# Optimization experiments

Measured on AMD Instinct MI355X. Metric: run time of the kernel, lower is better.

Reference implementation:

```python
import jax, jax.numpy as jnp
import numpy as np

HIDDEN = 1024
FFN = 4096
NUM_EXPERTS = 8
TOP_K = 2


def setup_inputs() -> dict:
    key = jax.random.key(0)
    k1, k2, k3, k4, k5 = jax.random.split(key, 5)
    B, T = 4, 2048
    x = jax.random.normal(k1, (B, T, HIDDEN), dtype=jnp.float32)
    # router: nn.Linear(hidden_dim, num_experts)
    bound = 1.0 / np.sqrt(HIDDEN)
    router_w = jax.random.uniform(k2, (NUM_EXPERTS, HIDDEN), dtype=jnp.float32, minval=-bound, maxval=bound)
    router_b = jax.random.uniform(k3, (NUM_EXPERTS,), dtype=jnp.float32, minval=-bound, maxval=bound)
    w1 = jax.random.normal(k4, (NUM_EXPERTS, HIDDEN, FFN), dtype=jnp.float32) * 0.02
    w2 = jax.random.normal(k5, (NUM_EXPERTS, FFN, HIDDEN), dtype=jnp.float32) * 0.02
    return {"x": x, "router_w": router_w, "router_b": router_b, "w1": w1, "w2": w2}


def reference(x, router_w, router_b, w1, w2):
    B, T, H = x.shape
    x_flat = x.reshape(-1, H)                      # [N, H], N = B*T
    logits = x_flat @ router_w.T + router_b        # [N, E]
    probs = jax.nn.softmax(logits, axis=-1)
    topk_w, topk_idx = jax.lax.top_k(probs, TOP_K)  # [N, K]
    topk_w = topk_w / jnp.sum(topk_w, axis=-1, keepdims=True)
    # combine weight per (expert, token): sum_k topk_w[:,k] * onehot(topk_idx[:,k])
    onehot = jax.nn.one_hot(topk_idx, NUM_EXPERTS, dtype=x.dtype)   # [N, K, E]
    combine = jnp.einsum('nk,nke->en', topk_w, onehot)              # [E, N]
    # dense per-expert FFN (math identical to original masked loop: gelu(0)=0)
    hidden = jax.nn.gelu(jnp.einsum('nh,ehf->enf', x_flat, w1), approximate=False)  # [E, N, F]
    expert_out = jnp.einsum('enf,efh->enh', hidden, w2)             # [E, N, H]
    out = jnp.einsum('enh,en->nh', expert_out, combine)             # [N, H]
    return out.reshape(B, T, H)
```

## Files before the change

### kernel.cpp

```cpp
#include <hip/hip_runtime.h>
#include <cstdint>
#include <cstddef>

#define H_DIM 1024
#define F_DIM 4096
#define N_EXP 8
#define N_TOK 8192
#define NK_ASSIGN (N_TOK * 2)
#define MAX_MB 24
#define NMB 32

typedef unsigned short u16;
typedef __attribute__((ext_vector_type(8))) short bf16x8;
typedef __attribute__((ext_vector_type(4))) float f32x4;

__device__ __forceinline__ u16 f2bf(float f) {
  unsigned int u = __float_as_uint(f);
  u += 0x7fffu + ((u >> 16) & 1u);
  return (u16)(u >> 16);
}

__device__ __forceinline__ void load16(const u16* g, u16* l) {
  __builtin_amdgcn_global_load_lds(
      (const __attribute__((address_space(1))) void*)g,
      (__attribute__((address_space(3))) void*)l, 16, 0, 0);
}

__global__ __launch_bounds__(256) void router_kernel(
    const float* __restrict__ x, const float* __restrict__ rw,
    const float* __restrict__ rb, int* __restrict__ topk_idx,
    float* __restrict__ topk_w, u16* __restrict__ xb) {
  const int lane = threadIdx.x & 63;
  const int wid = threadIdx.x >> 6;
  const int t = blockIdx.x * 4 + wid;
  const float4* xr = (const float4*)(x + (size_t)t * H_DIM);
  u16* xo = xb + (size_t)t * H_DIM;
  float acc[N_EXP];
#pragma unroll
  for (int e = 0; e < N_EXP; ++e) acc[e] = 0.f;
#pragma unroll
  for (int j = 0; j < 4; ++j) {
    float4 xv = xr[j * 64 + lane];
    ushort4 u;
    u.x = f2bf(xv.x); u.y = f2bf(xv.y); u.z = f2bf(xv.z); u.w = f2bf(xv.w);
    *(ushort4*)(xo + (size_t)(j * 64 + lane) * 4) = u;
#pragma unroll
    for (int e = 0; e < N_EXP; ++e) {
      float4 wv = ((const float4*)(rw + e * H_DIM))[j * 64 + lane];
      acc[e] += xv.x * wv.x + xv.y * wv.y + xv.z * wv.z + xv.w * wv.w;
    }
  }
#pragma unroll
  for (int off = 32; off > 0; off >>= 1) {
#pragma unroll
    for (int e = 0; e < N_EXP; ++e) acc[e] += __shfl_xor(acc[e], off);
  }
  if (lane == 0) {
    float lg[N_EXP];
#pragma unroll
    for (int e = 0; e < N_EXP; ++e) lg[e] = acc[e] + rb[e];
    int i0 = 0;
    float b0 = lg[0];
#pragma unroll
    for (int e = 1; e < N_EXP; ++e)
      if (lg[e] > b0) { b0 = lg[e]; i0 = e; }
    int i1 = -1;
    float b1 = -3.4e38f;
#pragma unroll
    for (int e = 0; e < N_EXP; ++e)
      if (e != i0 && lg[e] > b1) { b1 = lg[e]; i1 = e; }
    float w0 = 1.f / (1.f + __expf(b1 - b0));
    topk_idx[2 * t] = i0;
    topk_idx[2 * t + 1] = i1;
    topk_w[2 * t] = w0;
    topk_w[2 * t + 1] = 1.f - w0;
  }
}

__global__ __launch_bounds__(256) void hist_kernel(
    const int* __restrict__ topk_idx, int* __restrict__ hist_g) {
  __shared__ int hh[N_EXP];
  const int tid = threadIdx.x;
  if (tid < N_EXP) hh[tid] = 0;
  __syncthreads();
  const int t = blockIdx.x * 256 + tid;
  const int e0 = topk_idx[2 * t], e1 = topk_idx[2 * t + 1];
  atomicAdd(&hh[e0], 1);
  atomicAdd(&hh[e1], 1);
  __syncthreads();
  if (tid < N_EXP) hist_g[blockIdx.x * N_EXP + tid] = hh[tid];
}

__global__ __launch_bounds__(256) void scatter_kernel(
    const int* __restrict__ topk_idx, const float* __restrict__ topk_w,
    const int* __restrict__ hist_g, int* __restrict__ offsets,
    int* __restrict__ assign_token, float* __restrict__ assign_gate,
    int* __restrict__ slot_of) {
  __shared__ int sh[NMB * N_EXP];
  __shared__ int pb[N_EXP];
  __shared__ int cur[N_EXP];
  const int tid = threadIdx.x;
  sh[tid] = hist_g[tid];
  if (tid < N_EXP) cur[tid] = 0;
  __syncthreads();
  if (tid == 0) {
    int tot[N_EXP];
    for (int e = 0; e < N_EXP; ++e) tot[e] = 0;
    for (int b = 0; b < NMB; ++b)
      for (int e = 0; e < N_EXP; ++e) tot[e] += sh[b * N_EXP + e];
    int run = 0;
    for (int e = 0; e < N_EXP; ++e) {
      if (blockIdx.x == 0) offsets[e] = run;
      int r = run;
      for (int b = 0; b < (int)blockIdx.x; ++b) r += sh[b * N_EXP + e];
      pb[e] = r;
      run += tot[e];
    }
    if (blockIdx.x == 0) offsets[N_EXP] = run;
  }
  __syncthreads();
  const int t = blockIdx.x * 256 + tid;
#pragma unroll
  for (int k = 0; k < 2; ++k) {
    int e = topk_idx[2 * t + k];
    int local = atomicAdd(&cur[e], 1);
    int pos = pb[e] + local;
    assign_token[pos] = t;
    assign_gate[pos] = topk_w[2 * t + k];
    slot_of[2 * t + k] = pos;
  }
}

__global__ __launch_bounds__(256) void transpose_cvt(
    const float* __restrict__ in, u16* __restrict__ out, int R, int C) {
  __shared__ u16 lds[64 * 66];
  const int e = blockIdx.z;
  const float* ip = in + (size_t)e * R * C;
  u16* op = out + (size_t)e * R * C;
  const int c0 = blockIdx.x * 64, r0 = blockIdx.y * 64;
  const int tid = threadIdx.x;
  const int tx = tid & 15, ty = tid >> 4;
#pragma unroll
  for (int i = 0; i < 4; ++i) {
    const int r = ty + i * 16;
    float4 v = *(const float4*)(ip + (size_t)(r0 + r) * C + c0 + tx * 4);
    ushort2 u01, u23;
    u01.x = f2bf(v.x); u01.y = f2bf(v.y);
    u23.x = f2bf(v.z); u23.y = f2bf(v.w);
    *(ushort2*)&lds[r * 66 + tx * 4] = u01;
    *(ushort2*)&lds[r * 66 + tx * 4 + 2] = u23;
  }
  __syncthreads();
  const int lane = tid & 63, wid = tid >> 6;
  const int r8 = lane & 7;
#pragma unroll
  for (int s = 0; s < 2; ++s) {
    const int c = s * 32 + wid * 8 + (lane >> 3);
    union { u16 u[8]; uint4 q; } pk;
#pragma unroll
    for (int k = 0; k < 8; ++k) pk.u[k] = lds[(r8 * 8 + k) * 66 + c];
    *(uint4*)(op + (size_t)(c0 + c) * R + r0 + r8 * 8) = pk.q;
  }
}

template <int LDA, int LDB, int LDC, int KITERS, int NXB, bool FIRST>
__global__ __launch_bounds__(256) void moe_gemm(
    const u16* __restrict__ Abase, const u16* __restrict__ Bbase,
    u16* __restrict__ hout, float* __restrict__ yout,
    const int* __restrict__ offsets, const float* __restrict__ assign_gate,
    const int* __restrict__ atok) {
  __shared__ __align__(16) u16 As[128 * 64];
  __shared__ __align__(16) u16 Bs[128 * 64];
  const int flat = blockIdx.x + NXB * (blockIdx.y + MAX_MB * blockIdx.z);
  const int e = flat & 7;
  const int s = flat >> 3;
  const int mb = s % MAX_MB;
  const int n0b = s / MAX_MB;
  const int row0 = offsets[e];
  const int cnt = offsets[e + 1] - row0;
  const int mbase = mb * 128;
  if (mbase >= cnt) return;
  const int mrem = cnt - mbase;
  const int n0 = n0b * 128;
  const int tid = threadIdx.x;
  const int lane = tid & 63;
  const int wid = tid >> 6;
  const int wm = wid & 1, wn = wid >> 1;
  const u16* B = Bbase + (size_t)e * ((size_t)H_DIM * F_DIM);
  const int row16 = lane & 15, quad = lane >> 4;
  const int sr = lane >> 3;
  const int scol = ((lane & 7) ^ sr) * 8;

  const u16* Arow[4];
  const u16* Brow[4];
#pragma unroll
  for (int i = 0; i < 4; ++i) {
    const int c = wid * 4 + i;
    const int r = c * 8 + sr;
    const int ra = min(r, mrem - 1);
    if (FIRST) {
      const int tok = atok[row0 + mbase + ra];
      Arow[i] = Abase + (size_t)tok * LDA + scol;
    } else {
      Arow[i] = Abase + (size_t)(row0 + mbase + ra) * LDA + scol;
    }
    Brow[i] = B + (size_t)(n0 + r) * LDB + scol;
  }

  f32x4 acc[4][4];
#pragma unroll
  for (int i = 0; i < 4; ++i)
#pragma unroll
    for (int j = 0; j < 4; ++j)
#pragma unroll
      for (int r = 0; r < 4; ++r) acc[i][j][r] = 0.f;

  for (int kt = 0; kt < KITERS; ++kt) {
    const int k0 = kt * 64;
#pragma unroll
    for (int i = 0; i < 4; ++i) {
      const int c = wid * 4 + i;
      load16(Arow[i] + k0, &As[c * 512]);
      load16(Brow[i] + k0, &Bs[c * 512]);
    }
    __syncthreads();
#pragma unroll
    for (int ks = 0; ks < 2; ++ks) {
      bf16x8 av[4], bv[4];
#pragma unroll
      for (int mi = 0; mi < 4; ++mi) {
        const int r = wm * 64 + mi * 16 + row16;
        av[mi] = *(const bf16x8*)&As[r * 64 + ((ks * 4 + quad) ^ (r & 7)) * 8];
      }
#pragma unroll
      for (int ni = 0; ni < 4; ++ni) {
        const int r = wn * 64 + ni * 16 + row16;
        bv[ni] = *(const bf16x8*)&Bs[r * 64 + ((ks * 4 + quad) ^ (r & 7)) * 8];
      }
#pragma unroll
      for (int mi = 0; mi < 4; ++mi)
#pragma unroll
        for (int ni = 0; ni < 4; ++ni)
          acc[mi][ni] =
              __builtin_amdgcn_mfma_f32_16x16x32_bf16(av[mi], bv[ni], acc[mi][ni], 0, 0, 0);
    }
    __syncthreads();
  }

  if (FIRST) {
    u16* Cp = hout + (size_t)(row0 + mbase) * LDC + n0;
#pragma unroll
    for (int mi = 0; mi < 4; ++mi) {
#pragma unroll
      for (int r = 0; r < 4; ++r) {
        const int lm = wm * 64 + mi * 16 + quad * 4 + r;
        if (lm < mrem) {
#pragma unroll
          for (int ni = 0; ni < 4; ++ni) {
            float v = acc[mi][ni][r];
            float t = v * (0.7978845608028654f + 0.0356774081363f * v * v);
            v = v / (1.f + __expf(-2.f * t));
            Cp[(size_t)lm * LDC + (wn * 64 + ni * 16 + row16)] = f2bf(v);
          }
        }
      }
    }
  } else {
#pragma unroll
    for (int mi = 0; mi < 4; ++mi) {
#pragma unroll
      for (int r = 0; r < 4; ++r) {
        const int lm = wm * 64 + mi * 16 + quad * 4 + r;
        if (lm < mrem) {
          const int slot = row0 + mbase + lm;
          const float g = assign_gate[slot];
          float* orow = yout + (size_t)slot * LDC + n0;
#pragma unroll
          for (int ni = 0; ni < 4; ++ni)
            orow[wn * 64 + ni * 16 + row16] = acc[mi][ni][r] * g;
        }
      }
    }
  }
}

__global__ __launch_bounds__(256) void combine_kernel(
    const float* __restrict__ ys, const int* __restrict__ slot_of,
    float* __restrict__ out) {
  const int t = blockIdx.x;
  const int s0 = slot_of[2 * t], s1 = slot_of[2 * t + 1];
  const int i = threadIdx.x;
  float4 a = ((const float4*)(ys + (size_t)s0 * H_DIM))[i];
  float4 b = ((const float4*)(ys + (size_t)s1 * H_DIM))[i];
  float4 o;
  o.x = a.x + b.x; o.y = a.y + b.y; o.z = a.z + b.z; o.w = a.w + b.w;
  ((float4*)(out + (size_t)t * H_DIM))[i] = o;
}

extern "C" void kernel_launch(void* const* d_in, const int* in_sizes, int n_in,
                              void* d_out, int out_size, void* d_ws, size_t ws_size,
                              hipStream_t stream) {
  const float* x = (const float*)d_in[0];
  const float* rw = (const float*)d_in[1];
  const float* rb = (const float*)d_in[2];
  const float* w1 = (const float*)d_in[3];
  const float* w2 = (const float*)d_in[4];
  float* out = (float*)d_out;

  char* ws = (char*)d_ws;
  u16* w1b = (u16*)(ws);
  float* y_slot = (float*)(ws);
  u16* w2b = (u16*)(ws + 67108864);
  u16* xb = (u16*)(ws + 134217728);
  u16* h = (u16*)(ws + 167772160);
  int* hist_g = (int*)(ws + 167772160);
  char* meta = ws + 301989888;
  int* offsets = (int*)(meta + 64);
  int* topk_idx = (int*)(meta + 128);
  float* topk_w = (float*)(meta + 128 + 65536);
  int* assign_token = (int*)(meta + 128 + 131072);
  float* assign_gate = (float*)(meta + 128 + 196608);
  int* slot_of = (int*)(meta + 128 + 262144);

  router_kernel<<<N_TOK / 4, 256, 0, stream>>>(x, rw, rb, topk_idx, topk_w, xb);
  hist_kernel<<<NMB, 256, 0, stream>>>(topk_idx, hist_g);
  scatter_kernel<<<NMB, 256, 0, stream>>>(topk_idx, topk_w, hist_g, offsets,
                                          assign_token, assign_gate, slot_of);
  transpose_cvt<<<dim3(F_DIM / 64, H_DIM / 64, N_EXP), 256, 0, stream>>>(w1, w1b, H_DIM, F_DIM);
  transpose_cvt<<<dim3(H_DIM / 64, F_DIM / 64, N_EXP), 256, 0, stream>>>(w2, w2b, F_DIM, H_DIM);

  moe_gemm<H_DIM, H_DIM, F_DIM, H_DIM / 64, F_DIM / 128, true>
      <<<dim3(F_DIM / 128, MAX_MB, N_EXP), 256, 0, stream>>>(
          xb, w1b, h, nullptr, offsets, assign_gate, assign_token);
  moe_gemm<F_DIM, F_DIM, H_DIM, F_DIM / 64, H_DIM / 128, false>
      <<<dim3(H_DIM / 128, MAX_MB, N_EXP), 256, 0, stream>>>(
          h, w2b, nullptr, y_slot, offsets, assign_gate, nullptr);
  combine_kernel<<<N_TOK, 256, 0, stream>>>(y_slot, slot_of, out);

  (void)in_sizes; (void)n_in; (void)ws_size;
}
```

Measured before the change: 907.9 us.

## Double-buffer MoE GEMM LDS tiles with K=32 stages and vmcnt-based prefetch

After: 807.6 us. 11.0% less time.

```diff
diff --git a/kernel.cpp b/kernel.cpp
--- a/kernel.cpp
+++ b/kernel.cpp
@@ -169,8 +169,8 @@
     u16* __restrict__ hout, float* __restrict__ yout,
     const int* __restrict__ offsets, const float* __restrict__ assign_gate,
     const int* __restrict__ atok) {
-  __shared__ __align__(16) u16 As[128 * 64];
-  __shared__ __align__(16) u16 Bs[128 * 64];
+  __shared__ __align__(16) u16 As[2 * 128 * 32];
+  __shared__ __align__(16) u16 Bs[2 * 128 * 32];
   const int flat = blockIdx.x + NXB * (blockIdx.y + MAX_MB * blockIdx.z);
   const int e = flat & 7;
   const int s = flat >> 3;
@@ -188,15 +188,15 @@
   const int wm = wid & 1, wn = wid >> 1;
   const u16* B = Bbase + (size_t)e * ((size_t)H_DIM * F_DIM);
   const int row16 = lane & 15, quad = lane >> 4;
-  const int sr = lane >> 3;
-  const int scol = ((lane & 7) ^ sr) * 8;
-
-  const u16* Arow[4];
-  const u16* Brow[4];
-#pragma unroll
-  for (int i = 0; i < 4; ++i) {
-    const int c = wid * 4 + i;
-    const int r = c * 8 + sr;
+  const int srow = lane >> 2;
+  const int scol = (lane & 3) * 8;
+
+  const u16* Arow[2];
+  const u16* Brow[2];
+#pragma unroll
+  for (int i = 0; i < 2; ++i) {
+    const int c = wid * 2 + i;
+    const int r = c * 16 + srow;
     const int ra = min(r, mrem - 1);
     if (FIRST) {
       const int tok = atok[row0 + mbase + ra];
@@ -215,28 +215,36 @@
 #pragma unroll
       for (int r = 0; r < 4; ++r) acc[i][j][r] = 0.f;
 
+  auto stage = [&](int buf, int kt) {
+    const int k0 = kt * 32;
+#pragma unroll
+    for (int i = 0; i < 2; ++i) {
+      const int c = wid * 2 + i;
+      load16(Arow[i] + k0, &As[buf * 4096 + c * 512]);
+      load16(Brow[i] + k0, &Bs[buf * 4096 + c * 512]);
+    }
+  };
+
+  stage(0, 0);
+  int buf = 0;
+#pragma unroll 1
   for (int kt = 0; kt < KITERS; ++kt) {
-    const int k0 = kt * 64;
-#pragma unroll
-    for (int i = 0; i < 4; ++i) {
-      const int c = wid * 4 + i;
-      load16(Arow[i] + k0, &As[c * 512]);
-      load16(Brow[i] + k0, &Bs[c * 512]);
-    }
-    __syncthreads();
-#pragma unroll
-    for (int ks = 0; ks < 2; ++ks) {
+    const int ktn = (kt + 1 < KITERS) ? kt + 1 : kt;
+    stage(buf ^ 1, ktn);
+    asm volatile("s_waitcnt vmcnt(4)" ::: "memory");
+    __builtin_amdgcn_sched_barrier(0);
+    __builtin_amdgcn_s_barrier();
+    __builtin_amdgcn_sched_barrier(0);
+    {
+      const u16* Ab = As + buf * 4096;
+      const u16* Bb = Bs + buf * 4096;
       bf16x8 av[4], bv[4];
 #pragma unroll
-      for (int mi = 0; mi < 4; ++mi) {
-        const int r = wm * 64 + mi * 16 + row16;
-        av[mi] = *(const bf16x8*)&As[r * 64 + ((ks * 4 + quad) ^ (r & 7)) * 8];
-      }
-#pragma unroll
-      for (int ni = 0; ni < 4; ++ni) {
-        const int r = wn * 64 + ni * 16 + row16;
-        bv[ni] = *(const bf16x8*)&Bs[r * 64 + ((ks * 4 + quad) ^ (r & 7)) * 8];
-      }
+      for (int mi = 0; mi < 4; ++mi)
+        av[mi] = *(const bf16x8*)&Ab[(wm * 64 + mi * 16 + row16) * 32 + quad * 8];
+#pragma unroll
+      for (int ni = 0; ni < 4; ++ni)
+        bv[ni] = *(const bf16x8*)&Bb[(wn * 64 + ni * 16 + row16) * 32 + quad * 8];
 #pragma unroll
       for (int mi = 0; mi < 4; ++mi)
 #pragma unroll
@@ -244,8 +252,12 @@
           acc[mi][ni] =
               __builtin_amdgcn_mfma_f32_16x16x32_bf16(av[mi], bv[ni], acc[mi][ni], 0, 0, 0);
     }
-    __syncthreads();
-  }
+    __builtin_amdgcn_sched_barrier(0);
+    __builtin_amdgcn_s_barrier();
+    __builtin_amdgcn_sched_barrier(0);
+    buf ^= 1;
+  }
+  asm volatile("s_waitcnt vmcnt(0)" ::: "memory");
 
   if (FIRST) {
     u16* Cp = hout + (size_t)(row0 + mbase) * LDC + n0;
@@ -329,10 +341,10 @@
   transpose_cvt<<<dim3(F_DIM / 64, H_DIM / 64, N_EXP), 256, 0, stream>>>(w1, w1b, H_DIM, F_DIM);
   transpose_cvt<<<dim3(H_DIM / 64, F_DIM / 64, N_EXP), 256, 0, stream>>>(w2, w2b, F_DIM, H_DIM);
 
-  moe_gemm<H_DIM, H_DIM, F_DIM, H_DIM / 64, F_DIM / 128, true>
+  moe_gemm<H_DIM, H_DIM, F_DIM, H_DIM / 32, F_DIM / 128, true>
       <<<dim3(F_DIM / 128, MAX_MB, N_EXP), 256, 0, stream>>>(
           xb, w1b, h, nullptr, offsets, assign_gate, assign_token);
-  moe_gemm<F_DIM, F_DIM, H_DIM, F_DIM / 64, H_DIM / 128, false>
+  moe_gemm<F_DIM, F_DIM, H_DIM, F_DIM / 32, H_DIM / 128, false>
       <<<dim3(H_DIM / 128, MAX_MB, N_EXP), 256, 0, stream>>>(
           h, w2b, nullptr, y_slot, offsets, assign_gate, nullptr);
   combine_kernel<<<N_TOK, 256, 0, stream>>>(y_slot, slot_of, out);
```
